# Kernel optimization log

Hardware: AMD Instinct MI355X
Metric: run time of the kernel (lower is better)

## Reference

```python
import jax, jax.numpy as jnp
import numpy as np

IN_F, OUT_F, GROUP = 4096, 11008, 128
TOKENS = 64


def setup_inputs() -> dict:
    key = jax.random.key(0)
    k1, k2, k3, k4 = jax.random.split(key, 4)
    x = jax.random.normal(k1, (TOKENS, IN_F), dtype=jnp.float32).astype(jnp.float16)
    # packed uint8 values stored in int32 (two int4 nibbles per byte)
    w_packed = jax.random.randint(k2, (IN_F, OUT_F // 2), 0, 256, dtype=jnp.int32)
    num_groups = IN_F // GROUP
    w_scale = (jax.random.uniform(k3, (num_groups, OUT_F), minval=1e-3, maxval=0.1)).astype(jnp.float16)
    w_zero = jnp.round(jax.random.uniform(k4, (num_groups, OUT_F), minval=0.0, maxval=15.0)).astype(jnp.float16)
    return {"x": x, "w_packed": w_packed, "w_scale": w_scale, "w_zero": w_zero}


def _dequantize_int4(w_packed, w_scale, w_zero, group_size=GROUP):
    in_f = w_packed.shape[0]
    out_f = w_packed.shape[1] * 2
    w_low = (w_packed & 15).astype(jnp.float16)          # even output columns
    w_high = ((w_packed >> 4) & 15).astype(jnp.float16)  # odd output columns
    # interleave low/high -> [in_f, out_f]
    w_int4 = jnp.stack([w_low, w_high], axis=-1).reshape(in_f, out_f)
    num_groups = in_f // group_size
    w_g = w_int4.reshape(num_groups, group_size, out_f)
    w = (w_g - w_zero[:, None, :]) * w_scale[:, None, :]
    return w.reshape(in_f, out_f)


def reference(x, w_packed, w_scale, w_zero):
    w = _dequantize_int4(w_packed, w_scale, w_zero)  # [in_f, out_f] fp16
    return jnp.matmul(x.astype(jnp.float16), w)      # [tokens, out_f]
```

## Files before the change

### kernel.cpp

```cpp
#include <hip/hip_runtime.h>
#include <stdint.h>

#define IN_F   4096
#define OUT_F  11008
#define C32    5504
#define LDST   72
#define KSPL   4
#define KBLK   1024
#define NST    16
#define NGRP   8

typedef __attribute__((ext_vector_type(8))) _Float16 half8;
typedef __attribute__((ext_vector_type(4))) float floatx4;

static __device__ __forceinline__ uint32_t pkh(float a, float b) {
    auto h = __builtin_amdgcn_cvt_pkrtz(a, b);
    union { decltype(h) v; uint32_t u; } r; r.v = h; return r.u;
}

__global__ __launch_bounds__(256) void prep_kernel(
    const float* __restrict__ x, uint32_t* __restrict__ xh, float4* __restrict__ out4)
{
    int tid = blockIdx.x * 256 + threadIdx.x;
    if (tid < (64 * OUT_F / 4)) out4[tid] = make_float4(0.f, 0.f, 0.f, 0.f);
    if (tid < (64 * IN_F / 2)) {
        float2 v = ((const float2*)x)[tid];
        xh[tid] = pkh(v.x, v.y);
    }
}

__global__ __launch_bounds__(256, 8) void int4_gemm_kernel(
    const int*      __restrict__ wp,
    const float*    __restrict__ wscale,
    const float*    __restrict__ wzero,
    const uint32_t* __restrict__ xh,
    float*          __restrict__ out)
{
    __shared__ float4 tab[NGRP * 16];
    __shared__ __align__(16) ushort bld[2][32 * LDST];

    const int tid   = threadIdx.x;
    const int col0  = blockIdx.x * 32;
    const int ky    = blockIdx.y;
    const int kbase = ky * KBLK;

    const int c  = tid & 15;
    const int kb = (tid >> 4) * 4;
    const int ce = 2 * c, co = ce + 1;
    const int* wbase = wp + (size_t)(kbase + kb) * C32 + (col0 >> 1) + c;

    const int wave = tid >> 6;
    const int lane = tid & 63;
    const int g    = lane >> 4;
    const int bc0  = lane & 15;
    const int bc1  = bc0 + 16;
    const uint32_t* xbase = xh + (size_t)(wave * 16 + bc0) * (IN_F / 2) + (kbase >> 1) + g * 4;

    if (tid < NGRP * 16) {
        int gg = tid >> 4, cp = tid & 15;
        size_t b = (size_t)(ky * NGRP + gg) * OUT_F + col0 + 2 * cp;
        float se = wscale[b], so = wscale[b + 1];
        float ze = wzero[b],  zo = wzero[b + 1];
        tab[tid] = make_float4(se, ze * se, so, zo * so);
    }

    floatx4 acc0 = {0.f, 0.f, 0.f, 0.f}, acc1 = {0.f, 0.f, 0.f, 0.f};

    struct Pref { uint32_t q0, q1, q2, q3; };
    auto issue = [&](int st) {
        const int* p = wbase + (size_t)st * (64 * (size_t)C32);
        Pref P;
        P.q0 = (uint32_t)p[0];
        P.q1 = (uint32_t)p[C32];
        P.q2 = (uint32_t)p[2 * C32];
        P.q3 = (uint32_t)p[3 * C32];
        return P;
    };

    auto dq_write = [&](ushort* buf, const Pref& P, int st) {
        float4 t = tab[((st >> 1) << 4) + c];
        float l0 = fmaf((float)( P.q0        & 15u), t.x, -t.y);
        float l1 = fmaf((float)( P.q1        & 15u), t.x, -t.y);
        float l2 = fmaf((float)( P.q2        & 15u), t.x, -t.y);
        float l3 = fmaf((float)( P.q3        & 15u), t.x, -t.y);
        float h0 = fmaf((float)((P.q0 >> 4)  & 15u), t.z, -t.w);
        float h1 = fmaf((float)((P.q1 >> 4)  & 15u), t.z, -t.w);
        float h2 = fmaf((float)((P.q2 >> 4)  & 15u), t.z, -t.w);
        float h3 = fmaf((float)((P.q3 >> 4)  & 15u), t.z, -t.w);
        *(uint2*)(buf + ce * LDST + kb) = make_uint2(pkh(l0, l1), pkh(l2, l3));
        *(uint2*)(buf + co * LDST + kb) = make_uint2(pkh(h0, h1), pkh(h2, h3));
    };

    auto compute = [&](const ushort* buf, int st) {
        union { uint4 u; half8 h; } a0, a1;
        a0.u = *(const uint4*)(xbase + (size_t)st * 32);
        a1.u = *(const uint4*)(xbase + (size_t)st * 32 + 16);
        half8 B00 = *(const half8*)(buf + bc0 * LDST + g * 8);
        half8 B01 = *(const half8*)(buf + bc0 * LDST + 32 + g * 8);
        half8 B10 = *(const half8*)(buf + bc1 * LDST + g * 8);
        half8 B11 = *(const half8*)(buf + bc1 * LDST + 32 + g * 8);
        acc0 = __builtin_amdgcn_mfma_f32_16x16x32_f16(a0.h, B00, acc0, 0, 0, 0);
        acc1 = __builtin_amdgcn_mfma_f32_16x16x32_f16(a0.h, B10, acc1, 0, 0, 0);
        acc0 = __builtin_amdgcn_mfma_f32_16x16x32_f16(a1.h, B01, acc0, 0, 0, 0);
        acc1 = __builtin_amdgcn_mfma_f32_16x16x32_f16(a1.h, B11, acc1, 0, 0, 0);
    };

    Pref P = issue(0);
    __syncthreads();
    dq_write(bld[0], P, 0);
    P = issue(1);
    asm volatile("s_waitcnt lgkmcnt(0)");
    __builtin_amdgcn_s_barrier();

    #pragma unroll 2
    for (int st = 0; st < NST; ++st) {
        if (st + 1 < NST) {
            Pref Pn = (st + 2 < NST) ? issue(st + 2) : P;
            dq_write(bld[(st + 1) & 1], P, st + 1);
            P = Pn;
        }
        compute(bld[st & 1], st);
        asm volatile("s_waitcnt lgkmcnt(0)");
        __builtin_amdgcn_s_barrier();
    }

    const int ocol = col0 + bc0;
    const int rb   = wave * 16 + g * 4;
    #pragma unroll
    for (int r = 0; r < 4; ++r) {
        unsafeAtomicAdd(out + (size_t)(rb + r) * OUT_F + ocol,      acc0[r]);
        unsafeAtomicAdd(out + (size_t)(rb + r) * OUT_F + ocol + 16, acc1[r]);
    }
}

extern "C" void kernel_launch(void* const* d_in, const int* in_sizes, int n_in,
                              void* d_out, int out_size, void* d_ws, size_t ws_size,
                              hipStream_t stream) {
    const float* x      = (const float*)d_in[0];
    const int*   wp     = (const int*)  d_in[1];
    const float* wscale = (const float*)d_in[2];
    const float* wzero  = (const float*)d_in[3];
    float*       out    = (float*)d_out;
    uint32_t*    xh     = (uint32_t*)d_ws;
    (void)in_sizes; (void)n_in; (void)out_size; (void)ws_size;

    prep_kernel<<<dim3(688), dim3(256), 0, stream>>>(x, xh, (float4*)out);
    int4_gemm_kernel<<<dim3(344, KSPL), dim3(256), 0, stream>>>(wp, wscale, wzero, xh, out);
}
```

Baseline: 47.29 us.

## Deepen weight prefetch pipeline, preload activations into registers, double split-K

Doubles the split-K factor so each block covers a 512-long K slice, which doubles the grid and the number of atomic adds into the output. The full activation slice is now loaded into registers up front instead of being fetched from global memory at every stage. Weight loads are issued four stages ahead through a ring of prefetch registers instead of one stage ahead. The occupancy hint is lowered to three blocks per SM to leave room for the extra registers. The intent is to hide global-load latency, at the cost of higher register pressure and more atomic traffic.

```diff
diff --git a/kernel.cpp b/kernel.cpp
--- a/kernel.cpp
+++ b/kernel.cpp
@@ -5,10 +5,10 @@
 #define OUT_F  11008
 #define C32    5504
 #define LDST   72
-#define KSPL   4
-#define KBLK   1024
-#define NST    16
-#define NGRP   8
+#define KSPL   8
+#define KBLK   512
+#define NST    8
+#define NGRP   4
 
 typedef __attribute__((ext_vector_type(8))) _Float16 half8;
 typedef __attribute__((ext_vector_type(4))) float floatx4;
@@ -16,6 +16,12 @@
 static __device__ __forceinline__ uint32_t pkh(float a, float b) {
     auto h = __builtin_amdgcn_cvt_pkrtz(a, b);
     union { decltype(h) v; uint32_t u; } r; r.v = h; return r.u;
+}
+
+static __device__ __forceinline__ void pipe_barrier() {
+    asm volatile("s_waitcnt lgkmcnt(0)" ::: "memory");
+    __builtin_amdgcn_s_barrier();
+    __builtin_amdgcn_sched_barrier(0);
 }
 
 __global__ __launch_bounds__(256) void prep_kernel(
@@ -29,7 +35,7 @@
     }
 }
 
-__global__ __launch_bounds__(256, 8) void int4_gemm_kernel(
+__global__ __launch_bounds__(256, 3) void int4_gemm_kernel(
     const int*      __restrict__ wp,
     const float*    __restrict__ wscale,
     const float*    __restrict__ wzero,
@@ -55,6 +61,13 @@
     const int bc0  = lane & 15;
     const int bc1  = bc0 + 16;
     const uint32_t* xbase = xh + (size_t)(wave * 16 + bc0) * (IN_F / 2) + (kbase >> 1) + g * 4;
+
+    uint4 Areg[2 * NST];
+    #pragma unroll
+    for (int s = 0; s < NST; ++s) {
+        Areg[2 * s]     = *(const uint4*)(xbase + s * 32);
+        Areg[2 * s + 1] = *(const uint4*)(xbase + s * 32 + 16);
+    }
 
     if (tid < NGRP * 16) {
         int gg = tid >> 4, cp = tid & 15;
@@ -93,8 +106,8 @@
 
     auto compute = [&](const ushort* buf, int st) {
         union { uint4 u; half8 h; } a0, a1;
-        a0.u = *(const uint4*)(xbase + (size_t)st * 32);
-        a1.u = *(const uint4*)(xbase + (size_t)st * 32 + 16);
+        a0.u = Areg[2 * st];
+        a1.u = Areg[2 * st + 1];
         half8 B00 = *(const half8*)(buf + bc0 * LDST + g * 8);
         half8 B01 = *(const half8*)(buf + bc0 * LDST + 32 + g * 8);
         half8 B10 = *(const half8*)(buf + bc1 * LDST + g * 8);
@@ -105,23 +118,22 @@
         acc1 = __builtin_amdgcn_mfma_f32_16x16x32_f16(a1.h, B11, acc1, 0, 0, 0);
     };
 
-    Pref P = issue(0);
     __syncthreads();
-    dq_write(bld[0], P, 0);
-    P = issue(1);
-    asm volatile("s_waitcnt lgkmcnt(0)");
-    __builtin_amdgcn_s_barrier();
 
-    #pragma unroll 2
+    Pref Ps[4];
+    Ps[0] = issue(0); Ps[1] = issue(1); Ps[2] = issue(2); Ps[3] = issue(3);
+    dq_write(bld[0], Ps[0], 0);
+    Ps[0] = issue(4);
+    pipe_barrier();
+
+    #pragma unroll 4
     for (int st = 0; st < NST; ++st) {
         if (st + 1 < NST) {
-            Pref Pn = (st + 2 < NST) ? issue(st + 2) : P;
-            dq_write(bld[(st + 1) & 1], P, st + 1);
-            P = Pn;
+            dq_write(bld[(st + 1) & 1], Ps[(st + 1) & 3], st + 1);
+            if (st + 5 < NST) Ps[(st + 1) & 3] = issue(st + 5);
         }
         compute(bld[st & 1], st);
-        asm volatile("s_waitcnt lgkmcnt(0)");
-        __builtin_amdgcn_s_barrier();
+        pipe_barrier();
     }
 
     const int ocol = col0 + bc0;
```

New measurement: 101.7 us. +115.0%, slower.
